# Optimization experiments

Measured on AMD Instinct MI355X. Metric: run time of the kernel, lower is better.

## Reference

```python
import jax, jax.numpy as jnp
import numpy as np
from jax import lax

B, S, H, T = 64, 512, 768, 9


def setup_inputs() -> dict:
    key = jax.random.key(0)
    ks = jax.random.split(key, 7)
    hidden = jax.random.normal(ks[0], (B, S, H), dtype=jnp.float32)
    W = jax.random.normal(ks[1], (H, T), dtype=jnp.float32) * 0.02
    b = jax.random.normal(ks[2], (T,), dtype=jnp.float32) * 0.02
    start_trans = jax.random.normal(ks[3], (T,), dtype=jnp.float32) * 0.1
    end_trans = jax.random.normal(ks[4], (T,), dtype=jnp.float32) * 0.1
    trans = jax.random.normal(ks[5], (T, T), dtype=jnp.float32) * 0.1
    labels = jax.random.randint(ks[6], (B, S), 0, T, dtype=jnp.int64)
    return {"hidden": hidden, "W": W, "b": b, "start_trans": start_trans,
            "end_trans": end_trans, "trans": trans, "labels": labels}


def _crf_nll(emissions, labels, start_trans, end_trans, trans):
    # emissions: [B,S,T], labels: [B,S] int. mask = labels > -1 (torchcrf semantics).
    maskf = (labels > -1).astype(emissions.dtype)          # [B,S]
    tags = jnp.maximum(labels, 0)                          # safe indexing

    # ---- numerator: score of the gold path ----
    tags0 = tags[:, 0]                                     # [B]
    num0 = start_trans[tags0] + jnp.take_along_axis(emissions[:, 0], tags0[:, None], axis=1)[:, 0]

    em_t = jnp.swapaxes(emissions[:, 1:], 0, 1)            # [S-1,B,T]
    tg_t = jnp.swapaxes(tags[:, 1:], 0, 1)                 # [S-1,B]
    mk_t = jnp.swapaxes(maskf[:, 1:], 0, 1)                # [S-1,B]

    def num_step(carry, xs):
        score, prev = carry
        em, tg, mk = xs
        step = trans[prev, tg] + jnp.take_along_axis(em, tg[:, None], axis=1)[:, 0]
        score = score + step * mk
        prev = jnp.where(mk > 0, tg, prev)
        return (score, prev), None

    (num, last_tags), _ = lax.scan(num_step, (num0, tags0), (em_t, tg_t, mk_t))
    num = num + end_trans[last_tags]                       # [B]

    # ---- denominator: log-partition via forward algorithm (log-semiring scan) ----
    alpha0 = start_trans[None, :] + emissions[:, 0]        # [B,T]

    def den_step(alpha, xs):
        em, mk = xs
        new = jax.nn.logsumexp(alpha[:, :, None] + trans[None, :, :], axis=1) + em  # [B,T]
        alpha = jnp.where(mk[:, None] > 0, new, alpha)
        return alpha, None

    alpha, _ = lax.scan(den_step, alpha0, (em_t, mk_t))
    den = jax.nn.logsumexp(alpha + end_trans[None, :], axis=1)  # [B]

    # model returns -crf(...) with reduction='mean'  =>  mean NLL
    return jnp.mean(den - num)


def reference(hidden, W, b, start_trans, end_trans, trans, labels):
    # token-classification head: [B,S,H] @ [H,T] -> emissions [B,S,T]
    emissions = jnp.einsum('bsh,ht->bst', hidden, W) + b
    return _crf_nll(emissions, labels, start_trans, end_trans, trans)
```

## Files before the change

### kernel.cpp

```cpp
#include <hip/hip_runtime.h>

constexpr int Bn = 64, Sn = 512, Hn = 768, Tn = 9;
constexpr int EMS = 12;
constexpr int CHUNKS = 16, CLEN = 32;

__device__ __forceinline__ float lse9(const float* e) {
    float m01 = fmaxf(e[0], e[1]), m23 = fmaxf(e[2], e[3]);
    float m45 = fmaxf(e[4], e[5]), m67 = fmaxf(e[6], e[7]);
    float m = fmaxf(fmaxf(fmaxf(m01, m23), fmaxf(m45, m67)), e[8]);
    float s = 0.f;
#pragma unroll
    for (int k = 0; k < 9; ++k) s += __expf(e[k] - m);
    return m + __logf(s);
}

__global__ __launch_bounds__(256) void emis_kernel(
        const float* __restrict__ hidden, const float* __restrict__ W,
        const float* __restrict__ bias, float* __restrict__ em,
        int nrows, int nwaves) {
    const int lane = threadIdx.x & 63;
    const int wid  = blockIdx.x * (blockDim.x >> 6) + (threadIdx.x >> 6);
    float wr[3][4][9];
#pragma unroll
    for (int k = 0; k < 3; ++k)
#pragma unroll
        for (int c = 0; c < 4; ++c) {
            const int h = 4 * lane + 256 * k + c;
#pragma unroll
            for (int t = 0; t < 9; ++t) wr[k][c][t] = W[h * 9 + t];
        }
    for (int row = wid; row < nrows; row += nwaves) {
        const float4* hp = reinterpret_cast<const float4*>(hidden + (size_t)row * Hn);
        float4 v0 = hp[lane], v1 = hp[lane + 64], v2 = hp[lane + 128];
        const float hv[3][4] = {{v0.x, v0.y, v0.z, v0.w},
                                {v1.x, v1.y, v1.z, v1.w},
                                {v2.x, v2.y, v2.z, v2.w}};
        float acc[9];
#pragma unroll
        for (int t = 0; t < 9; ++t) acc[t] = 0.f;
#pragma unroll
        for (int k = 0; k < 3; ++k)
#pragma unroll
            for (int c = 0; c < 4; ++c)
#pragma unroll
                for (int t = 0; t < 9; ++t)
                    acc[t] = fmaf(hv[k][c], wr[k][c][t], acc[t]);
#pragma unroll
        for (int m = 1; m < 64; m <<= 1)
#pragma unroll
            for (int t = 0; t < 9; ++t) acc[t] += __shfl_xor(acc[t], m, 64);
        if (lane == 0) {
            float* o = em + (size_t)row * EMS;
#pragma unroll
            for (int t = 0; t < 9; ++t) o[t] = acc[t] + bias[t];
        }
    }
}

__global__ __launch_bounds__(128) void chunk_kernel(
        const float* __restrict__ em, const float* __restrict__ trans,
        const int* __restrict__ labels, float* __restrict__ Mws) {
    const int b = blockIdx.x / CHUNKS;
    const int c = blockIdx.x % CHUNKS;
    const int tid = threadIdx.x;
    const bool act = tid < 81;
    const int i = tid / 9, j = tid % 9;
    __shared__ float Mbuf[2][9][12];
    __shared__ float emch[CLEN][EMS];
    __shared__ int   labch[CLEN];
    const int s0 = c * CLEN;
    const float* emb = em + ((size_t)b * Sn + s0) * EMS;
    for (int idx = tid; idx < CLEN * EMS; idx += 128)
        (&emch[0][0])[idx] = emb[idx];
    if (tid < CLEN) labch[tid] = labels[b * Sn + s0 + tid];
    float tc[9], row[9];
    float nv = (i == j) ? 0.f : -1e30f;
    if (act) {
#pragma unroll
        for (int k = 0; k < 9; ++k) tc[k] = trans[k * 9 + j];
#pragma unroll
        for (int k = 0; k < 9; ++k) row[k] = (k == i) ? 0.f : -1e30f;
    }
    __syncthreads();
    const int sbeg = (c == 0) ? 1 : 0;
    for (int sl = sbeg; sl < CLEN; ++sl) {
        if (act) {
            float e[9];
#pragma unroll
            for (int k = 0; k < 9; ++k) e[k] = row[k] + tc[k];
            float cand = lse9(e) + emch[sl][j];
            if (labch[sl] > -1) nv = cand;
            Mbuf[sl & 1][i][j] = nv;
        }
        __syncthreads();
        if (act) {
#pragma unroll
            for (int k = 0; k < 9; ++k) row[k] = Mbuf[sl & 1][i][k];
        }
    }
    if (act) Mws[(size_t)(b * CHUNKS + c) * 81 + tid] = nv;
}

__global__ __launch_bounds__(128) void final_kernel(
        const float* __restrict__ em, const float* __restrict__ Mws,
        const float* __restrict__ start, const float* __restrict__ endt,
        const float* __restrict__ trans, const int* __restrict__ labels,
        float* __restrict__ out) {
    const int b = blockIdx.x, tid = threadIdx.x;
    __shared__ float Ml[CHUNKS][9][12];
    __shared__ float red[128];
    for (int idx = tid; idx < CHUNKS * 81; idx += 128) {
        int c = idx / 81, r = idx % 81;
        Ml[c][r / 9][r % 9] = Mws[(size_t)(b * CHUNKS + c) * 81 + r];
    }
    const int* lb = labels + b * Sn;
    float np = 0.f;
    for (int s = tid; s < Sn; s += 128) {
        if (s >= 1) {
            int l = lb[s];
            if (l > -1) {
                int tp = lb[s - 1]; tp = tp > -1 ? tp : 0;
                np += trans[tp * 9 + l] + em[((size_t)b * Sn + s) * EMS + l];
            }
        }
    }
    red[tid] = np;
    __syncthreads();
    for (int off = 64; off > 0; off >>= 1) {
        if (tid < off) red[tid] += red[tid + off];
        __syncthreads();
    }
    if (tid < 9) {
        const int j = tid;
        float alpha[9];
#pragma unroll
        for (int k = 0; k < 9; ++k)
            alpha[k] = start[k] + em[(size_t)b * Sn * EMS + k];
        for (int c = 0; c < CHUNKS; ++c) {
            float e[9];
#pragma unroll
            for (int k = 0; k < 9; ++k) e[k] = alpha[k] + Ml[c][k][j];
            float nv = lse9(e);
#pragma unroll
            for (int k = 0; k < 9; ++k) alpha[k] = __shfl(nv, k, 64);
        }
        if (j == 0) {
            float e[9];
#pragma unroll
            for (int k = 0; k < 9; ++k) e[k] = alpha[k] + endt[k];
            float den = lse9(e);
            int t0 = lb[0] > -1 ? lb[0] : 0;
            float num = red[0] + start[t0] + em[(size_t)b * Sn * EMS + t0];
            int lt = lb[Sn - 1] > -1 ? lb[Sn - 1] : 0;
            num += endt[lt];
            atomicAdd(out, (den - num) * (1.0f / Bn));
        }
    }
}

extern "C" void kernel_launch(void* const* d_in, const int* in_sizes, int n_in,
                              void* d_out, int out_size, void* d_ws, size_t ws_size,
                              hipStream_t stream) {
    const float* hidden = (const float*)d_in[0];
    const float* W      = (const float*)d_in[1];
    const float* bias   = (const float*)d_in[2];
    const float* start  = (const float*)d_in[3];
    const float* endt   = (const float*)d_in[4];
    const float* trans  = (const float*)d_in[5];
    const int*   labels = (const int*)d_in[6];
    float* out = (float*)d_out;

    float* em  = (float*)d_ws;
    float* Mws = em + (size_t)Bn * Sn * EMS;

    hipMemsetAsync(d_out, 0, sizeof(float), stream);

    const int nrows  = Bn * Sn;
    const int blocks = 1024;
    emis_kernel<<<blocks, 256, 0, stream>>>(hidden, W, bias, em, nrows, blocks * 4);
    chunk_kernel<<<Bn * CHUNKS, 128, 0, stream>>>(em, trans, labels, Mws);
    final_kernel<<<Bn, 128, 0, stream>>>(em, Mws, start, endt, trans, labels, out);
}
```

Before: 196.2 us.

## Fuse emission GEMV into chunk scan kernel and move numerator into it

```diff
diff --git a/kernel.cpp b/kernel.cpp
--- a/kernel.cpp
+++ b/kernel.cpp
@@ -2,7 +2,7 @@
 
 constexpr int Bn = 64, Sn = 512, Hn = 768, Tn = 9;
 constexpr int EMS = 12;
-constexpr int CHUNKS = 16, CLEN = 32;
+constexpr int CHUNKS = 32, CLEN = 16;
 
 __device__ __forceinline__ float lse9(const float* e) {
     float m01 = fmaxf(e[0], e[1]), m23 = fmaxf(e[2], e[3]);
@@ -14,65 +14,98 @@
     return m + __logf(s);
 }
 
-__global__ __launch_bounds__(256) void emis_kernel(
+__global__ __launch_bounds__(128) void fused_kernel(
         const float* __restrict__ hidden, const float* __restrict__ W,
-        const float* __restrict__ bias, float* __restrict__ em,
-        int nrows, int nwaves) {
-    const int lane = threadIdx.x & 63;
-    const int wid  = blockIdx.x * (blockDim.x >> 6) + (threadIdx.x >> 6);
-    float wr[3][4][9];
-#pragma unroll
-    for (int k = 0; k < 3; ++k)
-#pragma unroll
-        for (int c = 0; c < 4; ++c) {
-            const int h = 4 * lane + 256 * k + c;
-#pragma unroll
-            for (int t = 0; t < 9; ++t) wr[k][c][t] = W[h * 9 + t];
-        }
-    for (int row = wid; row < nrows; row += nwaves) {
-        const float4* hp = reinterpret_cast<const float4*>(hidden + (size_t)row * Hn);
-        float4 v0 = hp[lane], v1 = hp[lane + 64], v2 = hp[lane + 128];
-        const float hv[3][4] = {{v0.x, v0.y, v0.z, v0.w},
-                                {v1.x, v1.y, v1.z, v1.w},
-                                {v2.x, v2.y, v2.z, v2.w}};
-        float acc[9];
-#pragma unroll
-        for (int t = 0; t < 9; ++t) acc[t] = 0.f;
-#pragma unroll
-        for (int k = 0; k < 3; ++k)
-#pragma unroll
-            for (int c = 0; c < 4; ++c)
-#pragma unroll
-                for (int t = 0; t < 9; ++t)
-                    acc[t] = fmaf(hv[k][c], wr[k][c][t], acc[t]);
-#pragma unroll
-        for (int m = 1; m < 64; m <<= 1)
-#pragma unroll
-            for (int t = 0; t < 9; ++t) acc[t] += __shfl_xor(acc[t], m, 64);
-        if (lane == 0) {
-            float* o = em + (size_t)row * EMS;
-#pragma unroll
-            for (int t = 0; t < 9; ++t) o[t] = acc[t] + bias[t];
-        }
-    }
-}
-
-__global__ __launch_bounds__(128) void chunk_kernel(
-        const float* __restrict__ em, const float* __restrict__ trans,
-        const int* __restrict__ labels, float* __restrict__ Mws) {
+        const float* __restrict__ bias, const float* __restrict__ trans,
+        const int* __restrict__ labels,
+        float* __restrict__ Mws, float* __restrict__ numpart,
+        float* __restrict__ em0) {
+    __shared__ float Wl[Hn * Tn];
+    __shared__ float emch[CLEN][EMS];
+    __shared__ float Mbuf[2][9][12];
+    __shared__ int   labch[CLEN];
+
     const int b = blockIdx.x / CHUNKS;
     const int c = blockIdx.x % CHUNKS;
     const int tid = threadIdx.x;
+    const int lane = tid & 63;
+    const int wv = tid >> 6;
+
+    const float4* Wg4 = reinterpret_cast<const float4*>(W);
+    float4* Wl4 = reinterpret_cast<float4*>(Wl);
+    for (int idx = tid; idx < Hn * Tn / 4; idx += 128) Wl4[idx] = Wg4[idx];
+    if (tid < CLEN) labch[tid] = labels[b * Sn + c * CLEN + tid];
+    float br[9];
+#pragma unroll
+    for (int t = 0; t < 9; ++t) br[t] = bias[t];
+    __syncthreads();
+
+    const size_t hbase = ((size_t)b * Sn + (size_t)c * CLEN) * Hn;
+    const float4* hp0 = reinterpret_cast<const float4*>(hidden + hbase + (size_t)wv * Hn);
+    float4 pre0 = hp0[lane], pre1 = hp0[lane + 64], pre2 = hp0[lane + 128];
+
+    float wreg[3][36];
+#pragma unroll
+    for (int k = 0; k < 3; ++k) {
+        const float4* p = reinterpret_cast<const float4*>(&Wl[(4 * lane + 256 * k) * Tn]);
+#pragma unroll
+        for (int j = 0; j < 9; ++j) {
+            float4 q = p[j];
+            wreg[k][4 * j + 0] = q.x; wreg[k][4 * j + 1] = q.y;
+            wreg[k][4 * j + 2] = q.z; wreg[k][4 * j + 3] = q.w;
+        }
+    }
+
+    for (int r = wv; r < CLEN; r += 2) {
+        float4 v0 = pre0, v1 = pre1, v2 = pre2;
+        if (r + 2 < CLEN) {
+            const float4* hq = reinterpret_cast<const float4*>(hidden + hbase + (size_t)(r + 2) * Hn);
+            pre0 = hq[lane]; pre1 = hq[lane + 64]; pre2 = hq[lane + 128];
+        }
+        const float hv[12] = {v0.x, v0.y, v0.z, v0.w, v1.x, v1.y, v1.z, v1.w,
+                              v2.x, v2.y, v2.z, v2.w};
+        float acc[9];
+#pragma unroll
+        for (int t = 0; t < 9; ++t) acc[t] = 0.f;
+#pragma unroll
+        for (int k = 0; k < 3; ++k)
+#pragma unroll
+            for (int cc = 0; cc < 4; ++cc)
+#pragma unroll
+                for (int t = 0; t < 9; ++t)
+                    acc[t] = fmaf(hv[k * 4 + cc], wreg[k][cc * 9 + t], acc[t]);
+#pragma unroll
+        for (int m = 1; m < 64; m <<= 1)
+#pragma unroll
+            for (int t = 0; t < 9; ++t) acc[t] += __shfl_xor(acc[t], m, 64);
+        if (lane == 0) {
+#pragma unroll
+            for (int t = 0; t < 9; ++t) emch[r][t] = acc[t] + br[t];
+        }
+    }
+    __syncthreads();
+
+    if (tid < 64) {
+        float term = 0.f;
+        if (tid < CLEN) {
+            int sg = c * CLEN + tid;
+            if (sg >= 1) {
+                int l = labch[tid];
+                if (l > -1) {
+                    int lp = (tid > 0) ? labch[tid - 1] : labels[b * Sn + sg - 1];
+                    if (lp < 0) lp = 0;
+                    term = trans[lp * 9 + l] + emch[tid][l];
+                }
+            }
+        }
+#pragma unroll
+        for (int m = 1; m < 16; m <<= 1) term += __shfl_xor(term, m, 64);
+        if (tid == 0) numpart[b * CHUNKS + c] = term;
+        if (c == 0 && tid < 9) em0[b * EMS + tid] = emch[0][tid];
+    }
+
     const bool act = tid < 81;
     const int i = tid / 9, j = tid % 9;
-    __shared__ float Mbuf[2][9][12];
-    __shared__ float emch[CLEN][EMS];
-    __shared__ int   labch[CLEN];
-    const int s0 = c * CLEN;
-    const float* emb = em + ((size_t)b * Sn + s0) * EMS;
-    for (int idx = tid; idx < CLEN * EMS; idx += 128)
-        (&emch[0][0])[idx] = emb[idx];
-    if (tid < CLEN) labch[tid] = labels[b * Sn + s0 + tid];
     float tc[9], row[9];
     float nv = (i == j) ? 0.f : -1e30f;
     if (act) {
@@ -81,7 +114,6 @@
 #pragma unroll
         for (int k = 0; k < 9; ++k) row[k] = (k == i) ? 0.f : -1e30f;
     }
-    __syncthreads();
     const int sbeg = (c == 0) ? 1 : 0;
     for (int sl = sbeg; sl < CLEN; ++sl) {
         if (act) {
@@ -102,40 +134,29 @@
 }
 
 __global__ __launch_bounds__(128) void final_kernel(
-        const float* __restrict__ em, const float* __restrict__ Mws,
-        const float* __restrict__ start, const float* __restrict__ endt,
-        const float* __restrict__ trans, const int* __restrict__ labels,
+        const float* __restrict__ Mws, const float* __restrict__ numpart,
+        const float* __restrict__ em0, const float* __restrict__ start,
+        const float* __restrict__ endt, const int* __restrict__ labels,
         float* __restrict__ out) {
     const int b = blockIdx.x, tid = threadIdx.x;
     __shared__ float Ml[CHUNKS][9][12];
-    __shared__ float red[128];
+    __shared__ float nred;
     for (int idx = tid; idx < CHUNKS * 81; idx += 128) {
         int c = idx / 81, r = idx % 81;
         Ml[c][r / 9][r % 9] = Mws[(size_t)(b * CHUNKS + c) * 81 + r];
     }
-    const int* lb = labels + b * Sn;
-    float np = 0.f;
-    for (int s = tid; s < Sn; s += 128) {
-        if (s >= 1) {
-            int l = lb[s];
-            if (l > -1) {
-                int tp = lb[s - 1]; tp = tp > -1 ? tp : 0;
-                np += trans[tp * 9 + l] + em[((size_t)b * Sn + s) * EMS + l];
-            }
-        }
-    }
-    red[tid] = np;
+    if (tid < 64) {
+        float np = (tid < CHUNKS) ? numpart[b * CHUNKS + tid] : 0.f;
+#pragma unroll
+        for (int m = 1; m < 32; m <<= 1) np += __shfl_xor(np, m, 64);
+        if (tid == 0) nred = np;
+    }
     __syncthreads();
-    for (int off = 64; off > 0; off >>= 1) {
-        if (tid < off) red[tid] += red[tid + off];
-        __syncthreads();
-    }
     if (tid < 9) {
         const int j = tid;
         float alpha[9];
 #pragma unroll
-        for (int k = 0; k < 9; ++k)
-            alpha[k] = start[k] + em[(size_t)b * Sn * EMS + k];
+        for (int k = 0; k < 9; ++k) alpha[k] = start[k] + em0[b * EMS + k];
         for (int c = 0; c < CHUNKS; ++c) {
             float e[9];
 #pragma unroll
@@ -149,10 +170,10 @@
 #pragma unroll
             for (int k = 0; k < 9; ++k) e[k] = alpha[k] + endt[k];
             float den = lse9(e);
+            const int* lb = labels + b * Sn;
             int t0 = lb[0] > -1 ? lb[0] : 0;
-            float num = red[0] + start[t0] + em[(size_t)b * Sn * EMS + t0];
             int lt = lb[Sn - 1] > -1 ? lb[Sn - 1] : 0;
-            num += endt[lt];
+            float num = nred + start[t0] + em0[b * EMS + t0] + endt[lt];
             atomicAdd(out, (den - num) * (1.0f / Bn));
         }
     }
@@ -170,14 +191,12 @@
     const int*   labels = (const int*)d_in[6];
     float* out = (float*)d_out;
 
-    float* em  = (float*)d_ws;
-    float* Mws = em + (size_t)Bn * Sn * EMS;
+    float* numpart = (float*)d_ws;
+    float* em0     = numpart + Bn * CHUNKS;
+    float* Mws     = em0 + Bn * EMS;
 
     hipMemsetAsync(d_out, 0, sizeof(float), stream);
-
-    const int nrows  = Bn * Sn;
-    const int blocks = 1024;
-    emis_kernel<<<blocks, 256, 0, stream>>>(hidden, W, bias, em, nrows, blocks * 4);
-    chunk_kernel<<<Bn * CHUNKS, 128, 0, stream>>>(em, trans, labels, Mws);
-    final_kernel<<<Bn, 128, 0, stream>>>(em, Mws, start, endt, trans, labels, out);
-}
+    fused_kernel<<<Bn * CHUNKS, 128, 0, stream>>>(hidden, W, bias, trans, labels,
+                                                  Mws, numpart, em0);
+    final_kernel<<<Bn, 128, 0, stream>>>(Mws, numpart, em0, start, endt, labels, out);
+}
```

Result: no change. 195.2 us (-0.5%).

## Prefetch next hidden row, stage W via LDS, and halve CRF chunk length

Applied to the files above, without the earlier changes.

```diff
diff --git a/kernel.cpp b/kernel.cpp
--- a/kernel.cpp
+++ b/kernel.cpp
@@ -2,7 +2,8 @@
 
 constexpr int Bn = 64, Sn = 512, Hn = 768, Tn = 9;
 constexpr int EMS = 12;
-constexpr int CHUNKS = 16, CLEN = 32;
+constexpr int CHUNKS = 32, CLEN = 16;
+constexpr int WPAD = 776;
 
 __device__ __forceinline__ float lse9(const float* e) {
     float m01 = fmaxf(e[0], e[1]), m23 = fmaxf(e[2], e[3]);
@@ -14,27 +15,45 @@
     return m + __logf(s);
 }
 
-__global__ __launch_bounds__(256) void emis_kernel(
+__global__ __launch_bounds__(256, 1) void emis_kernel(
         const float* __restrict__ hidden, const float* __restrict__ W,
-        const float* __restrict__ bias, float* __restrict__ em,
-        int nrows, int nwaves) {
-    const int lane = threadIdx.x & 63;
-    const int wid  = blockIdx.x * (blockDim.x >> 6) + (threadIdx.x >> 6);
-    float wr[3][4][9];
+        const float* __restrict__ bias, float* __restrict__ em) {
+    __shared__ float Wt[Tn * WPAD];
+    const int tid = threadIdx.x;
+    const int lane = tid & 63;
+
+    for (int f = tid; f < Hn * Tn; f += 256) {
+        int h = f / 9, t = f - 9 * h;
+        Wt[t * WPAD + h] = W[f];
+    }
+    const float myb = (lane < 9) ? bias[lane] : 0.f;
+    __syncthreads();
+
+    float4 wq[27];
 #pragma unroll
-    for (int k = 0; k < 3; ++k)
+    for (int t = 0; t < 9; ++t)
 #pragma unroll
-        for (int c = 0; c < 4; ++c) {
-            const int h = 4 * lane + 256 * k + c;
-#pragma unroll
-            for (int t = 0; t < 9; ++t) wr[k][c][t] = W[h * 9 + t];
+        for (int k = 0; k < 3; ++k)
+            wq[t * 3 + k] = *reinterpret_cast<const float4*>(
+                &Wt[t * WPAD + 4 * lane + 256 * k]);
+
+    const int wid = blockIdx.x * 4 + (tid >> 6);
+    const int nw  = gridDim.x * 4;
+    const int nrows = Bn * Sn;
+
+    int row = wid;
+    const float4* hp = reinterpret_cast<const float4*>(hidden + (size_t)row * Hn);
+    float4 p0 = hp[lane], p1 = hp[lane + 64], p2 = hp[lane + 128];
+
+    for (; row < nrows; ) {
+        const int nxt = row + nw;
+        float4 c0 = p0, c1 = p1, c2 = p2;
+        if (nxt < nrows) {
+            const float4* hq = reinterpret_cast<const float4*>(hidden + (size_t)nxt * Hn);
+            p0 = hq[lane]; p1 = hq[lane + 64]; p2 = hq[lane + 128];
         }
-    for (int row = wid; row < nrows; row += nwaves) {
-        const float4* hp = reinterpret_cast<const float4*>(hidden + (size_t)row * Hn);
-        float4 v0 = hp[lane], v1 = hp[lane + 64], v2 = hp[lane + 128];
-        const float hv[3][4] = {{v0.x, v0.y, v0.z, v0.w},
-                                {v1.x, v1.y, v1.z, v1.w},
-                                {v2.x, v2.y, v2.z, v2.w}};
+        const float hv[12] = {c0.x, c0.y, c0.z, c0.w, c1.x, c1.y, c1.z, c1.w,
+                              c2.x, c2.y, c2.z, c2.w};
         float acc[9];
 #pragma unroll
         for (int t = 0; t < 9; ++t) acc[t] = 0.f;
@@ -44,16 +63,16 @@
             for (int c = 0; c < 4; ++c)
 #pragma unroll
                 for (int t = 0; t < 9; ++t)
-                    acc[t] = fmaf(hv[k][c], wr[k][c][t], acc[t]);
+                    acc[t] = fmaf(hv[4 * k + c], ((const float*)&wq[t * 3 + k])[c], acc[t]);
 #pragma unroll
         for (int m = 1; m < 64; m <<= 1)
 #pragma unroll
             for (int t = 0; t < 9; ++t) acc[t] += __shfl_xor(acc[t], m, 64);
-        if (lane == 0) {
-            float* o = em + (size_t)row * EMS;
+        float v = acc[0];
 #pragma unroll
-            for (int t = 0; t < 9; ++t) o[t] = acc[t] + bias[t];
-        }
+        for (int t = 1; t < 9; ++t) v = (lane == t) ? acc[t] : v;
+        if (lane < 9) em[(size_t)row * EMS + lane] = v + myb;
+        row = nxt;
     }
 }
 
@@ -174,10 +193,7 @@
     float* Mws = em + (size_t)Bn * Sn * EMS;
 
     hipMemsetAsync(d_out, 0, sizeof(float), stream);
-
-    const int nrows  = Bn * Sn;
-    const int blocks = 1024;
-    emis_kernel<<<blocks, 256, 0, stream>>>(hidden, W, bias, em, nrows, blocks * 4);
+    emis_kernel<<<1024, 256, 0, stream>>>(hidden, W, bias, em);
     chunk_kernel<<<Bn * CHUNKS, 128, 0, stream>>>(em, trans, labels, Mws);
     final_kernel<<<Bn, 128, 0, stream>>>(em, Mws, start, endt, trans, labels, out);
 }
```

Result: no change. 195.4 us (-0.4%).
